# Performance work log

Measured on AMD Instinct MI355X. Metric: run time of the kernel, lower is better.

## Reference

```python
import jax, jax.numpy as jnp
import numpy as np

EMB_DIM = 2048
HIDDEN_DIM = 8192
BATCH = 4
SEQ = 2048


def _kaiming_normal(key, out_f, in_f):
    # kaiming_normal_(mode='fan_in', nonlinearity='relu'): std = sqrt(2 / fan_in)
    std = np.sqrt(2.0 / in_f).astype(np.float32)
    return jax.random.normal(key, (out_f, in_f), dtype=jnp.float32) * std


def setup_inputs() -> dict:
    key = jax.random.key(0)
    kx, k1, k2, k3 = jax.random.split(key, 4)
    x = jax.random.normal(kx, (BATCH, SEQ, EMB_DIM), dtype=jnp.float32)
    w1 = _kaiming_normal(k1, HIDDEN_DIM, EMB_DIM)   # fc1.weight [hidden, emb]
    w2 = _kaiming_normal(k2, HIDDEN_DIM, EMB_DIM)   # fc2.weight [hidden, emb]
    w3 = _kaiming_normal(k3, EMB_DIM, HIDDEN_DIM)   # fc3.weight [emb, hidden]
    return {"x": x, "w1": w1, "w2": w2, "w3": w3, "scale_x": 1}


def reference(x, w1, w2, w3, scale_x):
    # fc1/fc2: x @ W.T  (no bias). scale_x is unused in the fp (calibration) path.
    gate = jnp.einsum('bse,he->bsh', x, w1)  # [B,S,H]
    up = jnp.einsum('bse,he->bsh', x, w2)    # [B,S,H]
    h = jax.nn.silu(gate) * up               # Custom_SiLU + Custom_ElementWiseMul
    out = jnp.einsum('bsh,eh->bse', h, w3)   # fc3 down-projection
    return out
```

## Files before the change

### kernel.cpp

```cpp
#include <hip/hip_runtime.h>
#include <hip/hip_bf16.h>

#define M_ROWS 8192
#define E_DIM  2048
#define H_DIM  8192

typedef __attribute__((ext_vector_type(8))) short bf16x8;
typedef __attribute__((ext_vector_type(4))) float f32x4;
typedef __attribute__((ext_vector_type(4))) unsigned int uint4v;

__device__ __forceinline__ unsigned short f2bf_rne(float x) {
  unsigned u = __builtin_bit_cast(unsigned, x);
  u += 0x7FFFu + ((u >> 16) & 1u);
  return (unsigned short)(u >> 16);
}

__global__ __launch_bounds__(256) void cvt4_f32_bf16(const float* __restrict__ s0, unsigned short* __restrict__ d0,
                                                     const float* __restrict__ s1, unsigned short* __restrict__ d1,
                                                     const float* __restrict__ s2, unsigned short* __restrict__ d2,
                                                     const float* __restrict__ s3, unsigned short* __restrict__ d3,
                                                     int n8) {
  int i = blockIdx.x * blockDim.x + threadIdx.x;
  if (i >= n8) return;
  const float* in = (blockIdx.y == 0) ? s0 : (blockIdx.y == 1) ? s1 : (blockIdx.y == 2) ? s2 : s3;
  unsigned short* out = (blockIdx.y == 0) ? d0 : (blockIdx.y == 1) ? d1 : (blockIdx.y == 2) ? d2 : d3;
  const float4* p = (const float4*)(in + (size_t)i * 8);
  float4 a = p[0];
  float4 b = p[1];
  union { unsigned short us[8]; uint4v v; } r;
  r.us[0] = f2bf_rne(a.x); r.us[1] = f2bf_rne(a.y);
  r.us[2] = f2bf_rne(a.z); r.us[3] = f2bf_rne(a.w);
  r.us[4] = f2bf_rne(b.x); r.us[5] = f2bf_rne(b.y);
  r.us[6] = f2bf_rne(b.z); r.us[7] = f2bf_rne(b.w);
  *(uint4v*)(out + (size_t)i * 8) = r.v;
}

__device__ __forceinline__ void gld_lds16(const unsigned short* g, unsigned short* l) {
  __builtin_amdgcn_global_load_lds(
      (const __attribute__((address_space(1))) unsigned int*)g,
      (__attribute__((address_space(3))) unsigned int*)l, 16, 0, 0);
}

#define VMCNT(n)   asm volatile("s_waitcnt vmcnt(" #n ")" ::: "memory")

template <int EPI>
__global__ __launch_bounds__(512, 2)
void gemm256(const unsigned short* __restrict__ A,
             const unsigned short* __restrict__ B,
             const unsigned short* __restrict__ B2,
             void* __restrict__ Cout,
             int M, int N, int K) {
  __shared__ unsigned short sh[65536];
  unsigned short* lAb = sh;
  unsigned short* lBb = sh + 32768;

  const int tid = threadIdx.x;
  const int lane = tid & 63;
  const int wave = tid >> 6;
  const int wr = wave >> 2;
  const int wc = wave & 3;
  const int wrow = wave >> 1;
  const int wcol = wave & 1;
  const int lr = lane & 15, lk = lane >> 4;

  const int gx = gridDim.x;
  const int wg = blockIdx.y * gx + blockIdx.x;
  int bcol, brow;
  if constexpr (EPI == 3) {
    const int xcd = wg & 7, idx = wg >> 3;
    bcol = xcd * 8 + (idx & 7);
    brow = idx >> 3;
  } else {
    const int nwg = gx * gridDim.y;
    const int swz = (wg & 7) * (nwg >> 3) + (wg >> 3);
    bcol = swz % gx;
    brow = swz / gx;
  }

  const unsigned short* Ag = A + (size_t)brow * 256 * K;
  const unsigned short* BgH0;
  const unsigned short* BgH1;
  if constexpr (EPI == 3) {
    BgH0 = B  + (size_t)bcol * 128 * K;
    BgH1 = B2 + (size_t)bcol * 128 * K;
  } else {
    BgH0 = B + (size_t)bcol * 256 * K;
    BgH1 = BgH0 + (size_t)128 * K;
  }

  f32x4 acc[8][4] = {};
  const int NT = K >> 6;
  const int NI = NT >> 1;

  auto stageH = [&](const unsigned short* gbase, unsigned short* ldsh) {
#pragma unroll
    for (int i = 0; i < 2; ++i) {
      int p = i * 4096 + tid * 8;
      int row = p >> 6;
      int lslot = ((p >> 3) & 7) ^ (row & 7);
      gld_lds16(gbase + (size_t)row * K + lslot * 8, ldsh + p);
    }
  };

  const int xsw = (lr & 7) << 3;
  bf16x8 af[8][2], bf[4][2], bu[4][2];

#define RD_PH1(LA, LB) \
  if constexpr (EPI == 3) { \
    _Pragma("unroll") for (int m = 0; m < 4; ++m) { \
      int r = wrow * 64 + m * 16 + lr; \
      af[m][0] = *(const bf16x8*)&LA[(r * 64 + lk * 8) ^ xsw]; \
      af[m][1] = *(const bf16x8*)&LA[(r * 64 + 32 + lk * 8) ^ xsw]; } \
    _Pragma("unroll") for (int n = 0; n < 2; ++n) { \
      int r = wcol * 64 + n * 16 + lr; \
      bf[n][0] = *(const bf16x8*)&LB[(r * 64 + lk * 8) ^ xsw]; \
      bf[n][1] = *(const bf16x8*)&LB[(r * 64 + 32 + lk * 8) ^ xsw]; } \
  } else { \
    _Pragma("unroll") for (int m = 0; m < 4; ++m) { \
      int r = wr * 128 + m * 16 + lr; \
      af[m][0] = *(const bf16x8*)&LA[(r * 64 + lk * 8) ^ xsw]; \
      af[m][1] = *(const bf16x8*)&LA[(r * 64 + 32 + lk * 8) ^ xsw]; } \
    _Pragma("unroll") for (int n = 0; n < 2; ++n) { \
      int r = wc * 64 + n * 16 + lr; \
      bf[n][0] = *(const bf16x8*)&LB[(r * 64 + lk * 8) ^ xsw]; \
      bf[n][1] = *(const bf16x8*)&LB[(r * 64 + 32 + lk * 8) ^ xsw]; } \
  }
#define RD_PH2(LB) \
  if constexpr (EPI == 3) { \
    _Pragma("unroll") for (int n = 2; n < 4; ++n) { \
      int r = wcol * 64 + n * 16 + lr; \
      bf[n][0] = *(const bf16x8*)&LB[(r * 64 + lk * 8) ^ xsw]; \
      bf[n][1] = *(const bf16x8*)&LB[(r * 64 + 32 + lk * 8) ^ xsw]; } \
  } else { \
    _Pragma("unroll") for (int n = 2; n < 4; ++n) { \
      int r = wc * 64 + n * 16 + lr; \
      bf[n][0] = *(const bf16x8*)&LB[(r * 64 + lk * 8) ^ xsw]; \
      bf[n][1] = *(const bf16x8*)&LB[(r * 64 + 32 + lk * 8) ^ xsw]; } \
  }
#define RD_PH3(LA, LB) \
  if constexpr (EPI == 3) { \
    _Pragma("unroll") for (int n = 0; n < 4; ++n) { \
      int r = wcol * 64 + n * 16 + lr; \
      bu[n][0] = *(const bf16x8*)&LB[8192 + ((r * 64 + lk * 8) ^ xsw)]; \
      bu[n][1] = *(const bf16x8*)&LB[8192 + ((r * 64 + 32 + lk * 8) ^ xsw)]; } \
  } else { \
    _Pragma("unroll") for (int m = 4; m < 8; ++m) { \
      int r = wr * 128 + m * 16 + lr; \
      af[m][0] = *(const bf16x8*)&LA[(r * 64 + lk * 8) ^ xsw]; \
      af[m][1] = *(const bf16x8*)&LA[(r * 64 + 32 + lk * 8) ^ xsw]; } \
  }
#define PH_CORE_BEGIN \
  __builtin_amdgcn_s_barrier(); \
  asm volatile("s_waitcnt lgkmcnt(0)" ::: "memory"); \
  __builtin_amdgcn_sched_barrier(0); \
  __builtin_amdgcn_s_setprio(1);
#define PH_CORE_END __builtin_amdgcn_s_setprio(0);
#define MF(ACC_M, AV, BV) \
  acc[ACC_M][n] = __builtin_amdgcn_mfma_f32_16x16x32_bf16(AV[ks], BV[ks], acc[ACC_M][n], 0, 0, 0);
#define PH_MFMA_Q(Q) \
  PH_CORE_BEGIN \
  if constexpr (EPI == 3) { \
    if constexpr (Q == 1) { _Pragma("unroll") for (int m = 0; m < 4; ++m) _Pragma("unroll") for (int n = 0; n < 2; ++n) _Pragma("unroll") for (int ks = 0; ks < 2; ++ks) MF(m, af[m], bf[n]) } \
    if constexpr (Q == 2) { _Pragma("unroll") for (int m = 0; m < 4; ++m) _Pragma("unroll") for (int n = 2; n < 4; ++n) _Pragma("unroll") for (int ks = 0; ks < 2; ++ks) MF(m, af[m], bf[n]) } \
    if constexpr (Q == 3) { _Pragma("unroll") for (int m = 0; m < 4; ++m) _Pragma("unroll") for (int n = 0; n < 2; ++n) _Pragma("unroll") for (int ks = 0; ks < 2; ++ks) MF(m + 4, af[m], bu[n]) } \
    if constexpr (Q == 4) { _Pragma("unroll") for (int m = 0; m < 4; ++m) _Pragma("unroll") for (int n = 2; n < 4; ++n) _Pragma("unroll") for (int ks = 0; ks < 2; ++ks) MF(m + 4, af[m], bu[n]) } \
  } else { \
    if constexpr (Q == 1) { _Pragma("unroll") for (int m = 0; m < 4; ++m) _Pragma("unroll") for (int n = 0; n < 2; ++n) _Pragma("unroll") for (int ks = 0; ks < 2; ++ks) MF(m, af[m], bf[n]) } \
    if constexpr (Q == 2) { _Pragma("unroll") for (int m = 0; m < 4; ++m) _Pragma("unroll") for (int n = 2; n < 4; ++n) _Pragma("unroll") for (int ks = 0; ks < 2; ++ks) MF(m, af[m], bf[n]) } \
    if constexpr (Q == 3) { _Pragma("unroll") for (int m = 4; m < 8; ++m) _Pragma("unroll") for (int n = 0; n < 2; ++n) _Pragma("unroll") for (int ks = 0; ks < 2; ++ks) MF(m, af[m], bf[n]) } \
    if constexpr (Q == 4) { _Pragma("unroll") for (int m = 4; m < 8; ++m) _Pragma("unroll") for (int n = 2; n < 4; ++n) _Pragma("unroll") for (int ks = 0; ks < 2; ++ks) MF(m, af[m], bf[n]) } \
  } \
  PH_CORE_END

  stageH(Ag, lAb);
  stageH(Ag + (size_t)128 * K, lAb + 8192);
  stageH(BgH0, lBb);
  stageH(BgH1, lBb + 8192);
  stageH(Ag + 64, lAb + 16384);
  stageH(Ag + (size_t)128 * K + 64, lAb + 16384 + 8192);
  stageH(BgH0 + 64, lBb + 16384);
  stageH(BgH1 + 64, lBb + 16384 + 8192);
  VMCNT(0);
  __builtin_amdgcn_s_barrier();

  const unsigned short* lA0 = lAb;
  const unsigned short* lB0 = lBb;
  const unsigned short* lA1 = lAb + 16384;
  const unsigned short* lB1 = lBb + 16384;

  for (int it = 0; it < NI; ++it) {
    const int t = it << 1;
    const size_t kT1 = (size_t)(t + 1) * 64;
    const size_t kS2 = (size_t)((t + 2 < NT) ? t + 2 : NT - 1) * 64;
    const size_t kS3 = (size_t)((t + 3 < NT) ? t + 3 : NT - 1) * 64;

    RD_PH1(lA0, lB0);
    if (it > 0) stageH(Ag + (size_t)128 * K + kT1, lAb + 16384 + 8192);
    asm volatile("s_waitcnt lgkmcnt(8)" ::: "memory");
    PH_MFMA_Q(1);
    __builtin_amdgcn_s_barrier();

    RD_PH2(lB0);
    PH_MFMA_Q(2);
    __builtin_amdgcn_s_barrier();

    RD_PH3(lA0, lB0);
    stageH(BgH0 + kS2, lBb);
    PH_MFMA_Q(3);
    __builtin_amdgcn_s_barrier();

    stageH(BgH1 + kS2, lBb + 8192);
    stageH(Ag + kS2, lAb);
    PH_MFMA_Q(4);
    VMCNT(6);
    __builtin_amdgcn_s_barrier();

    RD_PH1(lA1, lB1);
    stageH(Ag + (size_t)128 * K + kS2, lAb + 8192);
    asm volatile("s_waitcnt lgkmcnt(8)" ::: "memory");
    PH_MFMA_Q(1);
    __builtin_amdgcn_s_barrier();

    RD_PH2(lB1);
    PH_MFMA_Q(2);
    __builtin_amdgcn_s_barrier();

    RD_PH3(lA1, lB1);
    stageH(BgH0 + kS3, lBb + 16384);
    PH_MFMA_Q(3);
    __builtin_amdgcn_s_barrier();

    stageH(BgH1 + kS3, lBb + 16384 + 8192);
    stageH(Ag + kS3, lAb + 16384);
    PH_MFMA_Q(4);
    VMCNT(6);
    __builtin_amdgcn_s_barrier();
  }
  VMCNT(0);

#undef RD_PH1
#undef RD_PH2
#undef RD_PH3
#undef PH_CORE_BEGIN
#undef PH_CORE_END
#undef MF
#undef PH_MFMA_Q

  if constexpr (EPI == 3) {
    const int row0 = brow * 256 + wrow * 64 + lk * 4;
    const int col0 = bcol * 128 + wcol * 64 + lr;
#pragma unroll
    for (int m = 0; m < 4; ++m)
#pragma unroll
      for (int n = 0; n < 4; ++n)
#pragma unroll
        for (int j = 0; j < 4; ++j) {
          float g = acc[m][n][j];
          float u = acc[m + 4][n][j];
          float s = g / (1.0f + __expf(-g));
          ((unsigned short*)Cout)[(size_t)(row0 + m * 16 + j) * N + (col0 + n * 16)] =
              f2bf_rne(s * u);
        }
  } else {
    const int row0 = brow * 256 + wr * 128 + lk * 4;
    const int col0 = bcol * 256 + wc * 64 + lr;
#pragma unroll
    for (int m = 0; m < 8; ++m)
#pragma unroll
      for (int n = 0; n < 4; ++n)
#pragma unroll
        for (int j = 0; j < 4; ++j) {
          size_t idx = (size_t)(row0 + m * 16 + j) * N + (col0 + n * 16);
          ((float*)Cout)[idx] = acc[m][n][j];
        }
  }
}

extern "C" void kernel_launch(void* const* d_in, const int* in_sizes, int n_in,
                              void* d_out, int out_size, void* d_ws, size_t ws_size,
                              hipStream_t stream) {
  const float* x  = (const float*)d_in[0];
  const float* w1 = (const float*)d_in[1];
  const float* w2 = (const float*)d_in[2];
  const float* w3 = (const float*)d_in[3];
  float* out = (float*)d_out;

  const int M = M_ROWS, E = E_DIM, H = H_DIM;

  unsigned short* xb  = (unsigned short*)d_ws;
  unsigned short* w1b = xb + (size_t)M * E;
  unsigned short* w2b = w1b + (size_t)H * E;
  unsigned short* hb  = w2b + (size_t)H * E;

  const int n8 = (M * E) / 8;
  const size_t need_hoist = ((size_t)M * E + 2 * (size_t)H * E + (size_t)M * H + (size_t)E * H) * 2;

  if (ws_size >= need_hoist) {
    unsigned short* w3b = hb + (size_t)M * H;
    cvt4_f32_bf16<<<dim3(n8 / 256, 4), 256, 0, stream>>>(x, xb, w1, w1b, w2, w2b, w3, w3b, n8);
    gemm256<3><<<dim3(H / 128, M / 256), 512, 0, stream>>>(xb, w1b, w2b, hb, M, H, E);
    gemm256<0><<<dim3(E / 256, M / 256), 512, 0, stream>>>(hb, w3b, nullptr, out, M, E, H);
  } else {
    unsigned short* w3b = xb;
    cvt4_f32_bf16<<<dim3(n8 / 256, 3), 256, 0, stream>>>(x, xb, w1, w1b, w2, w2b, nullptr, nullptr, n8);
    gemm256<3><<<dim3(H / 128, M / 256), 512, 0, stream>>>(xb, w1b, w2b, hb, M, H, E);
    cvt4_f32_bf16<<<dim3(n8 / 256, 1), 256, 0, stream>>>(w3, w3b, nullptr, nullptr, nullptr, nullptr, nullptr, nullptr, n8);
    gemm256<0><<<dim3(E / 256, M / 256), 512, 0, stream>>>(hb, w3b, nullptr, out, M, E, H);
  }
}
```

Before: 768.1 us.

## Make gate/up GEMM persistent over column subtiles with cross-tile prefetch

The fused gate/up GEMM now launches 256 workgroups. Each one loops over 8 consecutive column panels for a fixed row block, so 2048 tile launches are replaced by 256 persistent blocks. Prefetch of the next panel's first K slices runs during the tail of the current panel, which hides the pipeline prologue and epilogue between tiles. The A row block is refetched for each panel, and the SiLU epilogue stores now sit inside the loop, where they may stall the pipeline or raise register pressure.

```diff
diff --git a/kernel.cpp b/kernel.cpp
--- a/kernel.cpp
+++ b/kernel.cpp
@@ -65,32 +65,33 @@
 
   const int gx = gridDim.x;
   const int wg = blockIdx.y * gx + blockIdx.x;
-  int bcol, brow;
+  const int NSUB = (EPI == 3) ? 8 : 1;
+  int bcol0, brow;
   if constexpr (EPI == 3) {
-    const int xcd = wg & 7, idx = wg >> 3;
-    bcol = xcd * 8 + (idx & 7);
-    brow = idx >> 3;
+    const int xcd = wg & 7;
+    brow = wg >> 3;
+    bcol0 = xcd * 8;
   } else {
     const int nwg = gx * gridDim.y;
     const int swz = (wg & 7) * (nwg >> 3) + (wg >> 3);
-    bcol = swz % gx;
+    bcol0 = swz % gx;
     brow = swz / gx;
   }
 
   const unsigned short* Ag = A + (size_t)brow * 256 * K;
-  const unsigned short* BgH0;
-  const unsigned short* BgH1;
-  if constexpr (EPI == 3) {
-    BgH0 = B  + (size_t)bcol * 128 * K;
-    BgH1 = B2 + (size_t)bcol * 128 * K;
-  } else {
-    BgH0 = B + (size_t)bcol * 256 * K;
-    BgH1 = BgH0 + (size_t)128 * K;
-  }
+  const unsigned short* AgH1 = Ag + (size_t)128 * K;
+
+  auto panelH0 = [&](int bc) {
+    return (EPI == 3) ? B + (size_t)bc * 128 * K : B + (size_t)bc * 256 * K;
+  };
+  auto panelH1 = [&](int bc) {
+    return (EPI == 3) ? B2 + (size_t)bc * 128 * K : B + (size_t)bc * 256 * K + (size_t)128 * K;
+  };
 
   f32x4 acc[8][4] = {};
   const int NT = K >> 6;
   const int NI = NT >> 1;
+  const int NTm = NT - 1;
 
   auto stageH = [&](const unsigned short* gbase, unsigned short* ldsh) {
 #pragma unroll
@@ -126,14 +127,10 @@
       bf[n][1] = *(const bf16x8*)&LB[(r * 64 + 32 + lk * 8) ^ xsw]; } \
   }
 #define RD_PH2(LB) \
-  if constexpr (EPI == 3) { \
+  { \
+    const int wcx = (EPI == 3) ? wcol : wc; \
     _Pragma("unroll") for (int n = 2; n < 4; ++n) { \
-      int r = wcol * 64 + n * 16 + lr; \
-      bf[n][0] = *(const bf16x8*)&LB[(r * 64 + lk * 8) ^ xsw]; \
-      bf[n][1] = *(const bf16x8*)&LB[(r * 64 + 32 + lk * 8) ^ xsw]; } \
-  } else { \
-    _Pragma("unroll") for (int n = 2; n < 4; ++n) { \
-      int r = wc * 64 + n * 16 + lr; \
+      int r = wcx * 64 + n * 16 + lr; \
       bf[n][0] = *(const bf16x8*)&LB[(r * 64 + lk * 8) ^ xsw]; \
       bf[n][1] = *(const bf16x8*)&LB[(r * 64 + 32 + lk * 8) ^ xsw]; } \
   }
@@ -172,15 +169,18 @@
   } \
   PH_CORE_END
 
-  stageH(Ag, lAb);
-  stageH(Ag + (size_t)128 * K, lAb + 8192);
-  stageH(BgH0, lBb);
-  stageH(BgH1, lBb + 8192);
-  stageH(Ag + 64, lAb + 16384);
-  stageH(Ag + (size_t)128 * K + 64, lAb + 16384 + 8192);
-  stageH(BgH0 + 64, lBb + 16384);
-  stageH(BgH1 + 64, lBb + 16384 + 8192);
-  VMCNT(0);
+  {
+    const unsigned short* P0 = panelH0(bcol0);
+    const unsigned short* P1 = panelH1(bcol0);
+    stageH(Ag, lAb);
+    stageH(AgH1, lAb + 8192);
+    stageH(P0, lBb);
+    stageH(P1, lBb + 8192);
+    stageH(Ag + 64, lAb + 16384);
+    stageH(P0 + 64, lBb + 16384);
+    stageH(P1 + 64, lBb + 16384 + 8192);
+  }
+  VMCNT(6);
   __builtin_amdgcn_s_barrier();
 
   const unsigned short* lA0 = lAb;
@@ -188,53 +188,104 @@
   const unsigned short* lA1 = lAb + 16384;
   const unsigned short* lB1 = lBb + 16384;
 
-  for (int it = 0; it < NI; ++it) {
-    const int t = it << 1;
-    const size_t kT1 = (size_t)(t + 1) * 64;
-    const size_t kS2 = (size_t)((t + 2 < NT) ? t + 2 : NT - 1) * 64;
-    const size_t kS3 = (size_t)((t + 3 < NT) ? t + 3 : NT - 1) * 64;
-
-    RD_PH1(lA0, lB0);
-    if (it > 0) stageH(Ag + (size_t)128 * K + kT1, lAb + 16384 + 8192);
-    asm volatile("s_waitcnt lgkmcnt(8)" ::: "memory");
-    PH_MFMA_Q(1);
-    __builtin_amdgcn_s_barrier();
-
-    RD_PH2(lB0);
-    PH_MFMA_Q(2);
-    __builtin_amdgcn_s_barrier();
-
-    RD_PH3(lA0, lB0);
-    stageH(BgH0 + kS2, lBb);
-    PH_MFMA_Q(3);
-    __builtin_amdgcn_s_barrier();
-
-    stageH(BgH1 + kS2, lBb + 8192);
-    stageH(Ag + kS2, lAb);
-    PH_MFMA_Q(4);
-    VMCNT(6);
-    __builtin_amdgcn_s_barrier();
-
-    RD_PH1(lA1, lB1);
-    stageH(Ag + (size_t)128 * K + kS2, lAb + 8192);
-    asm volatile("s_waitcnt lgkmcnt(8)" ::: "memory");
-    PH_MFMA_Q(1);
-    __builtin_amdgcn_s_barrier();
-
-    RD_PH2(lB1);
-    PH_MFMA_Q(2);
-    __builtin_amdgcn_s_barrier();
-
-    RD_PH3(lA1, lB1);
-    stageH(BgH0 + kS3, lBb + 16384);
-    PH_MFMA_Q(3);
-    __builtin_amdgcn_s_barrier();
-
-    stageH(BgH1 + kS3, lBb + 16384 + 8192);
-    stageH(Ag + kS3, lAb + 16384);
-    PH_MFMA_Q(4);
-    VMCNT(6);
-    __builtin_amdgcn_s_barrier();
+  for (int sub = 0; sub < NSUB; ++sub) {
+    const int bcol = bcol0 + sub;
+    const unsigned short* BgH0 = panelH0(bcol);
+    const unsigned short* BgH1 = panelH1(bcol);
+    const int nsub = (sub + 1 < NSUB) ? sub + 1 : sub;
+    const unsigned short* BgH0n = panelH0(bcol0 + nsub);
+    const unsigned short* BgH1n = panelH1(bcol0 + nsub);
+
+    for (int it = 0; it < NI; ++it) {
+      const int t = it << 1;
+      const size_t kT1 = (size_t)(t + 1) * 64;
+      const bool o2 = (t + 2 >= NT);
+      const bool o3 = (t + 3 >= NT);
+      const size_t k2 = (size_t)((t + 2) & NTm) * 64;
+      const size_t k3 = (size_t)((t + 3) & NTm) * 64;
+      const unsigned short* B0s2 = (o2 ? BgH0n : BgH0) + k2;
+      const unsigned short* B1s2 = (o2 ? BgH1n : BgH1) + k2;
+      const unsigned short* B0s3 = (o3 ? BgH0n : BgH0) + k3;
+      const unsigned short* B1s3 = (o3 ? BgH1n : BgH1) + k3;
+
+      RD_PH1(lA0, lB0);
+      stageH(AgH1 + kT1, lAb + 16384 + 8192);
+      asm volatile("s_waitcnt lgkmcnt(8)" ::: "memory");
+      PH_MFMA_Q(1);
+      __builtin_amdgcn_s_barrier();
+
+      RD_PH2(lB0);
+      PH_MFMA_Q(2);
+      __builtin_amdgcn_s_barrier();
+
+      RD_PH3(lA0, lB0);
+      stageH(B0s2, lBb);
+      PH_MFMA_Q(3);
+      __builtin_amdgcn_s_barrier();
+
+      stageH(B1s2, lBb + 8192);
+      stageH(Ag + k2, lAb);
+      PH_MFMA_Q(4);
+      VMCNT(6);
+      __builtin_amdgcn_s_barrier();
+
+      RD_PH1(lA1, lB1);
+      stageH(AgH1 + k2, lAb + 8192);
+      asm volatile("s_waitcnt lgkmcnt(8)" ::: "memory");
+      PH_MFMA_Q(1);
+      __builtin_amdgcn_s_barrier();
+
+      RD_PH2(lB1);
+      PH_MFMA_Q(2);
+      __builtin_amdgcn_s_barrier();
+
+      RD_PH3(lA1, lB1);
+      stageH(B0s3, lBb + 16384);
+      PH_MFMA_Q(3);
+      __builtin_amdgcn_s_barrier();
+
+      stageH(B1s3, lBb + 16384 + 8192);
+      stageH(Ag + k3, lAb + 16384);
+      PH_MFMA_Q(4);
+      VMCNT(6);
+      __builtin_amdgcn_s_barrier();
+    }
+
+    if constexpr (EPI == 3) {
+      const int row0 = brow * 256 + wrow * 64 + lk * 4;
+      const int col0 = bcol * 128 + wcol * 64 + lr;
+#pragma unroll
+      for (int m = 0; m < 4; ++m)
+#pragma unroll
+        for (int n = 0; n < 4; ++n)
+#pragma unroll
+          for (int j = 0; j < 4; ++j) {
+            float g = acc[m][n][j];
+            float u = acc[m + 4][n][j];
+            float s = g / (1.0f + __expf(-g));
+            ((unsigned short*)Cout)[(size_t)(row0 + m * 16 + j) * N + (col0 + n * 16)] =
+                f2bf_rne(s * u);
+          }
+      if (sub + 1 < NSUB) {
+#pragma unroll
+        for (int m = 0; m < 8; ++m)
+#pragma unroll
+          for (int n = 0; n < 4; ++n)
+            acc[m][n] = f32x4{0.f, 0.f, 0.f, 0.f};
+      }
+    } else {
+      const int row0 = brow * 256 + wr * 128 + lk * 4;
+      const int col0 = bcol * 256 + wc * 64 + lr;
+#pragma unroll
+      for (int m = 0; m < 8; ++m)
+#pragma unroll
+        for (int n = 0; n < 4; ++n)
+#pragma unroll
+          for (int j = 0; j < 4; ++j) {
+            size_t idx = (size_t)(row0 + m * 16 + j) * N + (col0 + n * 16);
+            ((float*)Cout)[idx] = acc[m][n][j];
+          }
+    }
   }
   VMCNT(0);
 
@@ -245,35 +296,6 @@
 #undef PH_CORE_END
 #undef MF
 #undef PH_MFMA_Q
-
-  if constexpr (EPI == 3) {
-    const int row0 = brow * 256 + wrow * 64 + lk * 4;
-    const int col0 = bcol * 128 + wcol * 64 + lr;
-#pragma unroll
-    for (int m = 0; m < 4; ++m)
-#pragma unroll
-      for (int n = 0; n < 4; ++n)
-#pragma unroll
-        for (int j = 0; j < 4; ++j) {
-          float g = acc[m][n][j];
-          float u = acc[m + 4][n][j];
-          float s = g / (1.0f + __expf(-g));
-          ((unsigned short*)Cout)[(size_t)(row0 + m * 16 + j) * N + (col0 + n * 16)] =
-              f2bf_rne(s * u);
-        }
-  } else {
-    const int row0 = brow * 256 + wr * 128 + lk * 4;
-    const int col0 = bcol * 256 + wc * 64 + lr;
-#pragma unroll
-    for (int m = 0; m < 8; ++m)
-#pragma unroll
-      for (int n = 0; n < 4; ++n)
-#pragma unroll
-        for (int j = 0; j < 4; ++j) {
-          size_t idx = (size_t)(row0 + m * 16 + j) * N + (col0 + n * 16);
-          ((float*)Cout)[idx] = acc[m][n][j];
-        }
-  }
 }
 
 extern "C" void kernel_launch(void* const* d_in, const int* in_sizes, int n_in,
@@ -298,12 +320,12 @@
   if (ws_size >= need_hoist) {
     unsigned short* w3b = hb + (size_t)M * H;
     cvt4_f32_bf16<<<dim3(n8 / 256, 4), 256, 0, stream>>>(x, xb, w1, w1b, w2, w2b, w3, w3b, n8);
-    gemm256<3><<<dim3(H / 128, M / 256), 512, 0, stream>>>(xb, w1b, w2b, hb, M, H, E);
+    gemm256<3><<<dim3(256), 512, 0, stream>>>(xb, w1b, w2b, hb, M, H, E);
     gemm256<0><<<dim3(E / 256, M / 256), 512, 0, stream>>>(hb, w3b, nullptr, out, M, E, H);
   } else {
     unsigned short* w3b = xb;
     cvt4_f32_bf16<<<dim3(n8 / 256, 3), 256, 0, stream>>>(x, xb, w1, w1b, w2, w2b, nullptr, nullptr, n8);
-    gemm256<3><<<dim3(H / 128, M / 256), 512, 0, stream>>>(xb, w1b, w2b, hb, M, H, E);
+    gemm256<3><<<dim3(256), 512, 0, stream>>>(xb, w1b, w2b, hb, M, H, E);
     cvt4_f32_bf16<<<dim3(n8 / 256, 1), 256, 0, stream>>>(w3, w3b, nullptr, nullptr, nullptr, nullptr, nullptr, nullptr, n8);
     gemm256<0><<<dim3(E / 256, M / 256), 512, 0, stream>>>(hb, w3b, nullptr, out, M, E, H);
   }
```

Result: slower. 783.6 us (+2.0%).
